# Kernel optimization log

Measured on AMD Instinct MI355X. Metric: run time of the kernel, lower is better.

## Reference

```python
import jax, jax.numpy as jnp
import numpy as np

EPS_LN = 1e-5

def layer_norm(x, w, b):
    u = x.mean(-1, keepdims=True)
    s = jnp.mean((x - u) ** 2, -1, keepdims=True)
    return w * ((x - u) / jnp.sqrt(s + EPS_LN)) + b

def mlp(x, W, b, lw, lb):
    return jax.nn.relu(layer_norm(x @ W + b, lw, lb))

def mlp_gate(x, W, b, lw, lb):
    return jax.nn.sigmoid(layer_norm(x @ W + b, lw, lb))

def setup_inputs() -> dict:
    N, D = 768, 64
    key = jax.random.key(0)
    ks = jax.random.split(key, 12)
    inp = {
        'corr_index': jax.random.normal(ks[0], (N, N, 2), jnp.float32),
        'nei_index': jax.random.randint(ks[1], (N, N), 0, 2).astype(jnp.int64),
        'nei_num': jax.random.randint(ks[2], (N,), 0, N).astype(jnp.int64),
        'hidden_state': jax.random.normal(ks[3], (N, D), jnp.float32),
        'agent_v': jax.random.normal(ks[4], (N, 2), jnp.float32),
        # relativeLayer: MLP(3, D)
        'rel_w': jax.random.normal(ks[5], (3, D), jnp.float32) * (1.0 / np.sqrt(3)),
        'rel_b': jnp.zeros((D,), jnp.float32),
        'rel_lw': jnp.ones((D,), jnp.float32),
        'rel_lb': jnp.zeros((D,), jnp.float32),
        # ngate: MLP_gate(3D, D)
        'ng_w': jax.random.normal(ks[6], (3 * D, D), jnp.float32) * (1.0 / np.sqrt(3 * D)),
        'ng_b': jnp.zeros((D,), jnp.float32),
        'ng_lw': jnp.ones((D,), jnp.float32),
        'ng_lb': jnp.zeros((D,), jnp.float32),
        # WAr: MLP(3D, 1) -- LayerNorm(1) is identity in the source
        'war_w': jax.random.normal(ks[7], (3 * D, 1), jnp.float32) * (1.0 / np.sqrt(3 * D)),
        'war_b': jnp.zeros((1,), jnp.float32),
        # weight: MLP(D, D)
        'wt_w': jax.random.normal(ks[8], (D, D), jnp.float32) * (1.0 / np.sqrt(D)),
        'wt_b': jnp.zeros((D,), jnp.float32),
        'wt_lw': jnp.ones((D,), jnp.float32),
        'wt_lb': jnp.zeros((D,), jnp.float32),
    }
    return inp

def reference(corr_index, nei_index, nei_num, hidden_state, agent_v,
              rel_w, rel_b, rel_lw, rel_lb,
              ng_w, ng_b, ng_lw, ng_lb,
              war_w, war_b,
              wt_w, wt_b, wt_lw, wt_lb):
    N, D = hidden_state.shape
    # pair layout: row i*N+j  (i = receiver row of the NxN grid, j = column)
    agent_vt = jnp.tile(agent_v, (N, 1))                     # [N*N, 2], row i*N+j -> agent_v[j]
    corr_t = corr_index.reshape(N * N, 2)
    dot = agent_vt[:, 0] * corr_t[:, 0] + agent_vt[:, 1] * corr_t[:, 1]
    judge = jnp.sum(agent_vt ** 2, -1)
    angle = dot / (jnp.sqrt(judge * jnp.sum(corr_t ** 2, -1)) + 1e-10)
    angle = jnp.where(judge == 0, -1.0, angle)
    corr3 = jnp.concatenate([corr_t, angle[:, None]], -1)    # [N*N, 3]

    r_t = mlp(corr3, rel_w, rel_b, rel_lw, rel_lb)           # [N*N, D]
    nei_inputs = jnp.tile(hidden_state, (N, 1))              # row i*N+j -> h[j]
    hi_t = jnp.repeat(hidden_state, N, axis=0)               # row i*N+j -> h[i]
    tmp = jnp.concatenate([r_t, hi_t, nei_inputs], 1)        # [N*N, 3D]

    mask = (nei_index.reshape(N * N) > 0)
    nGate = mlp_gate(tmp, ng_w, ng_b, ng_lw, ng_lb)          # [N*N, D]
    tt = jax.nn.relu(tmp @ war_w + war_b).reshape(-1)        # LayerNorm(1) == identity

    Pos = jnp.where(mask, tt, 0.0).reshape(N, N)
    Pos = jnp.where(Pos == 0, -10000.0, Pos)
    Pos = jax.nn.softmax(Pos, axis=1)
    Pos_t = Pos.reshape(-1)

    H = jnp.where(mask[:, None], nei_inputs * nGate * Pos_t[:, None], 0.0)
    H_sum = mlp(H.reshape(N, N, D).sum(1), wt_w, wt_b, wt_lw, wt_lb)
    return hidden_state + H_sum
```

## Files before the change

kernel.cpp:

```cpp
#include <hip/hip_runtime.h>
#include <math.h>

#define NN 768
#define DD 64
#define WPB 4
#define TPW (NN / 16 / WPB)
#define RSTRIDE 34
#define PREBLKS 18

typedef _Float16 half8 __attribute__((ext_vector_type(8)));
typedef float    f32x4 __attribute__((ext_vector_type(4)));
typedef __fp16   p2f   __attribute__((ext_vector_type(2)));

union FragU { uint4 u4; unsigned int u[4]; half8 h; };
union PkU   { unsigned int u; p2f p; };

__device__ __forceinline__ unsigned int pk2(float a, float b) {
    PkU t; t.p = __builtin_amdgcn_cvt_pkrtz(a, b); return t.u;
}
__device__ __forceinline__ float lane_bcast(float v, int src) {
    return __int_as_float(__builtin_amdgcn_readlane(__float_as_int(v), src));
}
__device__ __forceinline__ f32x4 mfma16(FragU a, FragU b, f32x4 c) {
    return __builtin_amdgcn_mfma_f32_16x16x32_f16(a.h, b.h, c, 0, 0, 0);
}

__global__ __launch_bounds__(256) void k_prepack(
    const float* __restrict__ hs, const float* __restrict__ ng_w,
    const float* __restrict__ ng_b, const float* __restrict__ war_w,
    const float* __restrict__ war_b,
    const float* __restrict__ rel_w, const float* __restrict__ rel_b,
    const float* __restrict__ rel_lw, const float* __restrict__ rel_lb,
    float* __restrict__ sbase, float* __restrict__ warb, float* __restrict__ war3,
    unsigned int* __restrict__ hf16,
    unsigned int* __restrict__ afragS, unsigned int* __restrict__ afragR,
    float* __restrict__ mom)
{
    const int t = threadIdx.x, blk = blockIdx.x;
    const int lane = t & 63, q = t >> 6, g = lane >> 4, c16 = lane & 15;

    if (blk >= PREBLKS) {
        const int row = (blk - PREBLKS) * 4 + q;
        const float hv = hs[row * DD + lane];
        float a2 = ng_b[lane];
        #pragma unroll 8
        for (int k = 0; k < DD; ++k)
            a2 = fmaf(lane_bcast(hv, k), ng_w[(DD + k) * DD + lane], a2);
        sbase[row * DD + lane] = a2;
        float t2 = hv * war_w[DD + lane];
        float t3 = hv * war_w[2 * DD + lane];
        #pragma unroll
        for (int o = 32; o; o >>= 1) { t2 += __shfl_xor(t2, o); t3 += __shfl_xor(t3, o); }
        if (lane == 0) { warb[row] = t2 + war_b[0]; war3[row] = t3; }
        return;
    }

    for (int idx = blk * 256 + t; idx < NN * 32; idx += PREBLKS * 256) {
        const int row = idx >> 5, c = idx & 31;
        hf16[idx] = pk2(hs[row * DD + 2 * c], hs[row * DD + 2 * c + 1]);
    }

    if (blk < 16) {
        const int b = blk >> 2, c = blk & 3;
        const int dout = 16 * b + c16;
        const int k0 = 32 * c + g * 8 + 2 * q;
        const int r0 = (k0 < 64) ? k0 : (k0 + 64);
        afragS[(blk * 64 + lane) * 4 + q] =
            pk2(ng_w[r0 * DD + dout], ng_w[(r0 + 1) * DD + dout]);
    } else if (blk == 16) {
        const int b = q;
        const int d = 16 * b + c16;
        const float rlwd = rel_lw[d], rlbd = rel_lb[d];
        const float c0 = rel_w[d] * rlwd;
        const float c1 = rel_w[DD + d] * rlwd;
        const float c2 = rel_w[2 * DD + d] * rlwd;
        const float c3 = rel_b[d] * rlwd;
        PkU h01, h23, h45;
        h01.p = __builtin_amdgcn_cvt_pkrtz(c0, c1);
        h23.p = __builtin_amdgcn_cvt_pkrtz(c2, c3);
        h45.p = __builtin_amdgcn_cvt_pkrtz(rlwd, rlbd);
        const unsigned l01 = pk2(c0 - (float)h01.p[0], c1 - (float)h01.p[1]);
        const unsigned l23 = pk2(c2 - (float)h23.p[0], c3 - (float)h23.p[1]);
        const unsigned l45 = pk2(rlwd - (float)h45.p[0], rlbd - (float)h45.p[1]);
        const unsigned int base = (b * 64 + lane) * 4;
        unsigned v0, v1, v2;
        if (g == 0 || g == 1)      { v0 = h01.u; v1 = h23.u; v2 = h45.u; }
        else if (g == 2)           { v0 = l01;   v1 = l23;   v2 = l45;   }
        else                       { v0 = 0u;    v1 = 0u;    v2 = 0u;    }
        afragR[base + 0] = v0;
        afragR[base + 1] = v1;
        afragR[base + 2] = v2;
        afragR[base + 3] = 0u;
    } else {
        if (t < 64) {
            const float x0 = rel_w[t], x1 = rel_w[DD + t], x2 = rel_w[2 * DD + t];
            const float x3 = rel_b[t];
            float v[14] = {x0, x1, x2, x3,
                           x0 * x0, x1 * x1, x2 * x2, x3 * x3,
                           x0 * x1, x0 * x2, x0 * x3, x1 * x2, x1 * x3, x2 * x3};
            #pragma unroll
            for (int qq = 0; qq < 14; ++qq) {
                float s = v[qq];
                #pragma unroll
                for (int o = 32; o; o >>= 1) s += __shfl_xor(s, o);
                if (t == 0) mom[qq] = s * (1.f / 64.f);
            }
        }
    }
}

__global__ __launch_bounds__(64 * WPB) void k_main(
    const float* __restrict__ corr, const int* __restrict__ nei,
    const float* __restrict__ hs, const float* __restrict__ av,
    const float* __restrict__ ng_lw, const float* __restrict__ ng_lb,
    const float* __restrict__ war_w,
    const float* __restrict__ sbase, const float* __restrict__ warb,
    const float* __restrict__ war3,
    const unsigned int* __restrict__ afragS, const unsigned int* __restrict__ afragR,
    const unsigned int* __restrict__ hf16, const float* __restrict__ mom,
    const float* __restrict__ wt_w, const float* __restrict__ wt_b,
    const float* __restrict__ wt_lw, const float* __restrict__ wt_lb,
    float* __restrict__ out)
{
    const int i = blockIdx.x;
    const int tid = threadIdx.x;
    const int lane = tid & 63, wave = tid >> 6;
    const int g = lane >> 4, c16 = lane & 15;

    __shared__ uint4 aSlds[16 * 64];
    __shared__ unsigned int smr[WPB * 16 * RSTRIDE];
    __shared__ float sm_red[WPB][DD];
    __shared__ float sm_m[WPB], sm_l[WPB];

    #pragma unroll
    for (int idx = tid; idx < 16 * 64; idx += 64 * WPB)
        aSlds[idx] = ((const uint4*)afragS)[idx];
    __syncthreads();

    FragU aR[4];
    #pragma unroll
    for (int b = 0; b < 4; ++b) aR[b].u4 = ((const uint4*)afragR)[b * 64 + lane];

    float sb[16], nlwv[16], nlbv[16], wv16[16];
    #pragma unroll
    for (int b = 0; b < 4; ++b)
        #pragma unroll
        for (int r = 0; r < 4; ++r) {
            const int dout = 16 * b + g * 4 + r;
            sb[b * 4 + r]   = sbase[i * DD + dout];
            nlwv[b * 4 + r] = ng_lw[dout];
            nlbv[b * 4 + r] = ng_lb[dout];
            wv16[b * 4 + r] = war_w[dout];
        }

    const float m0 = mom[0], m1 = mom[1], m2 = mom[2], m3 = mom[3];
    const float M00 = mom[4], M11 = mom[5], M22 = mom[6], M33 = mom[7];
    const float M01 = mom[8], M02 = mom[9], M03 = mom[10];
    const float M12 = mom[11], M13 = mom[12], M23 = mom[13];

    const float warbase = warb[i];
    unsigned int* wrbase = smr + (wave * 16 + c16) * RSTRIDE;

    float acc[16];
    #pragma unroll
    for (int x = 0; x < 16; ++x) acc[x] = 0.f;
    float mrun = -INFINITY, lrun = 0.f;

    int jj = 16 * wave + c16;
    float2 cc = ((const float2*)corr)[i * NN + jj];
    float2 vv = ((const float2*)av)[jj];
    int    nv = nei[i * NN + jj];
    float  w3 = war3[jj];
    FragU bx2, bx3;
    bx2.u4 = *(const uint4*)(hf16 + jj * 32 + 4 * g);
    bx3.u4 = *(const uint4*)(hf16 + jj * 32 + 16 + 4 * g);

    #pragma unroll 1
    for (int t = 0; t < TPW; ++t) {
        const f32x4 hv0 = *(const f32x4*)(hs + jj * DD +  0 + 4 * g);
        const f32x4 hv1 = *(const f32x4*)(hs + jj * DD + 16 + 4 * g);
        const f32x4 hv2 = *(const f32x4*)(hs + jj * DD + 32 + 4 * g);
        const f32x4 hv3 = *(const f32x4*)(hs + jj * DD + 48 + 4 * g);

        const int tn  = (t + 1 < TPW) ? (t + 1) : t;
        const int jjn = 16 * (wave + WPB * tn) + c16;
        const float2 cc_n = ((const float2*)corr)[i * NN + jjn];
        const float2 vv_n = ((const float2*)av)[jjn];
        const int    nv_n = nei[i * NN + jjn];
        const float  w3_n = war3[jjn];
        FragU bx2_n, bx3_n;
        bx2_n.u4 = *(const uint4*)(hf16 + jjn * 32 + 4 * g);
        bx3_n.u4 = *(const uint4*)(hf16 + jjn * 32 + 16 + 4 * g);

        const float cx = cc.x, cy = cc.y;
        const float judge = vv.x * vv.x + vv.y * vv.y;
        const float dotv = fmaf(vv.x, cx, vv.y * cy);
        const float cn = cx * cx + cy * cy;
        float angle = __fdividef(dotv, sqrtf(judge * cn) + 1e-10f);
        if (judge == 0.f) angle = -1.f;

        const float u = fmaf(cx, m0, fmaf(cy, m1, fmaf(angle, m2, m3)));
        float e2 = M33;
        e2 = fmaf(cx * cx, M00, e2);
        e2 = fmaf(cy * cy, M11, e2);
        e2 = fmaf(angle * angle, M22, e2);
        e2 = fmaf(2.f * cx, fmaf(cy, M01, fmaf(angle, M02, M03)), e2);
        e2 = fmaf(2.f * cy, fmaf(angle, M12, M13), e2);
        e2 = fmaf(2.f * angle, M23, e2);
        const float vare = (e2 - u * u) + 1e-5f;
        const float inv = rsqrtf(vare);
        const float sig = vare * inv;

        PkU s01, s23, s45;
        s01.p = __builtin_amdgcn_cvt_pkrtz(cx, cy);
        s23.p = __builtin_amdgcn_cvt_pkrtz(angle, 1.f);
        s45.p = __builtin_amdgcn_cvt_pkrtz(-u, sig);
        const unsigned l0 = pk2(cx - (float)s01.p[0], cy - (float)s01.p[1]);
        const unsigned l1 = pk2(angle - (float)s23.p[0], 0.f);
        const unsigned l2 = pk2((-u) - (float)s45.p[0], sig - (float)s45.p[1]);
        FragU b1;
        b1.u[0] = (g == 3) ? 0u : ((g == 1) ? l0 : s01.u);
        b1.u[1] = (g == 3) ? 0u : ((g == 1) ? l1 : s23.u);
        b1.u[2] = (g == 3) ? 0u : ((g == 1) ? l2 : s45.u);
        b1.u[3] = 0u;

        const f32x4 Z = {0.f, 0.f, 0.f, 0.f};
        float wd = 0.f;
        #pragma unroll
        for (int b = 0; b < 4; ++b) {
            const f32x4 P = mfma16(aR[b], b1, Z);
            const float r0f = fmaxf(P[0], 0.f) * inv;
            const float r1f = fmaxf(P[1], 0.f) * inv;
            const float r2f = fmaxf(P[2], 0.f) * inv;
            const float r3f = fmaxf(P[3], 0.f) * inv;
            wd = fmaf(r0f, wv16[b * 4 + 0], wd);
            wd = fmaf(r1f, wv16[b * 4 + 1], wd);
            wd = fmaf(r2f, wv16[b * 4 + 2], wd);
            wd = fmaf(r3f, wv16[b * 4 + 3], wd);
            uint2 wv;
            wv.x = pk2(r0f, r1f);
            wv.y = pk2(r2f, r3f);
            *(uint2*)(wrbase + 8 * b + 2 * g) = wv;
        }
        wd += __shfl_xor(wd, 16);
        wd += __shfl_xor(wd, 32);

        FragU bx0, bx1;
        {
            const uint2 lo0 = *(const uint2*)(wrbase + 4 * g);
            const uint2 hi0 = *(const uint2*)(wrbase + 4 * g + 2);
            bx0.u[0] = lo0.x; bx0.u[1] = lo0.y; bx0.u[2] = hi0.x; bx0.u[3] = hi0.y;
            const uint2 lo1 = *(const uint2*)(wrbase + 16 + 4 * g);
            const uint2 hi1 = *(const uint2*)(wrbase + 16 + 4 * g + 2);
            bx1.u[0] = lo1.x; bx1.u[1] = lo1.y; bx1.u[2] = hi1.x; bx1.u[3] = hi1.y;
        }

        f32x4 S[4];
        #pragma unroll
        for (int b = 0; b < 4; ++b) {
            FragU a0, a1, a2, a3;
            a0.u4 = aSlds[(b * 4 + 0) * 64 + lane];
            a1.u4 = aSlds[(b * 4 + 1) * 64 + lane];
            a2.u4 = aSlds[(b * 4 + 2) * 64 + lane];
            a3.u4 = aSlds[(b * 4 + 3) * 64 + lane];
            f32x4 cinit = {sb[b * 4 + 0], sb[b * 4 + 1], sb[b * 4 + 2], sb[b * 4 + 3]};
            cinit = mfma16(a0, bx0, cinit);
            cinit = mfma16(a1, bx1, cinit);
            cinit = mfma16(a2, bx2, cinit);
            cinit = mfma16(a3, bx3, cinit);
            S[b] = cinit;
        }

        float s1 = 0.f, s2 = 0.f;
        #pragma unroll
        for (int x = 0; x < 16; ++x) {
            const float sv = S[x >> 2][x & 3];
            s1 += sv; s2 = fmaf(sv, sv, s2);
        }
        s1 += __shfl_xor(s1, 16); s1 += __shfl_xor(s1, 32);
        s2 += __shfl_xor(s2, 16); s2 += __shfl_xor(s2, 32);
        const float u2 = s1 * (1.f / 64.f);
        const float var2 = fmaf(s2, 1.f / 64.f, -u2 * u2);
        const float inv2 = rsqrtf(var2 + 1e-5f);

        float tt = wd + w3 + warbase;
        tt = fmaxf(tt, 0.f);
        const bool msk = nv > 0;
        const float p = (msk && tt > 0.f) ? tt : -10000.f;

        float pm = p;
        pm = fmaxf(pm, __shfl_xor(pm, 1));
        pm = fmaxf(pm, __shfl_xor(pm, 2));
        pm = fmaxf(pm, __shfl_xor(pm, 4));
        pm = fmaxf(pm, __shfl_xor(pm, 8));
        const float mn = fmaxf(mrun, pm);
        const float alpha = __expf(mrun - mn);
        const float e = __expf(p - mn);
        const float eacc = msk ? e : 0.f;
        lrun = fmaf(lrun, alpha, e);
        mrun = mn;

        #pragma unroll
        for (int b = 0; b < 4; ++b) {
            const f32x4 hvb = (b == 0) ? hv0 : (b == 1) ? hv1 : (b == 2) ? hv2 : hv3;
            #pragma unroll
            for (int r = 0; r < 4; ++r) {
                const float ngv = fmaf((S[b][r] - u2) * inv2, nlwv[b * 4 + r],
                                       nlbv[b * 4 + r]);
                const float gate = __fdividef(1.f, 1.f + __expf(-ngv));
                acc[b * 4 + r] = fmaf(acc[b * 4 + r], alpha, eacc * gate * hvb[r]);
            }
        }

        jj = jjn; cc = cc_n; vv = vv_n; nv = nv_n; w3 = w3_n;
        bx2 = bx2_n; bx3 = bx3_n;
    }

    #pragma unroll
    for (int o = 1; o <= 8; o <<= 1) {
        lrun += __shfl_xor(lrun, o);
        #pragma unroll
        for (int x = 0; x < 16; ++x) acc[x] += __shfl_xor(acc[x], o);
    }
    if (c16 == 0) {
        #pragma unroll
        for (int b = 0; b < 4; ++b)
            #pragma unroll
            for (int r = 0; r < 4; ++r)
                sm_red[wave][16 * b + g * 4 + r] = acc[b * 4 + r];
        if (lane == 0) { sm_m[wave] = mrun; sm_l[wave] = lrun; }
    }
    __syncthreads();

    if (tid < DD) {
        float M = sm_m[0];
        #pragma unroll
        for (int w = 1; w < WPB; ++w) M = fmaxf(M, sm_m[w]);
        float L = 0.f, A = 0.f;
        #pragma unroll
        for (int w = 0; w < WPB; ++w) {
            const float f = __expf(sm_m[w] - M);
            L = fmaf(sm_l[w], f, L);
            A = fmaf(sm_red[w][tid], f, A);
        }
        const float Hv = A / L;
        float v = wt_b[tid];
        #pragma unroll 8
        for (int k = 0; k < DD; ++k)
            v = fmaf(lane_bcast(Hv, k), wt_w[k * DD + tid], v);
        float t1 = v, t2 = v * v;
        #pragma unroll
        for (int o = 32; o; o >>= 1) { t1 += __shfl_xor(t1, o); t2 += __shfl_xor(t2, o); }
        const float uo = t1 * (1.f / 64.f);
        const float varo = fmaf(t2, 1.f / 64.f, -uo * uo);
        const float invo = rsqrtf(varo + 1e-5f);
        const float ro = fmaf((v - uo) * invo, wt_lw[tid], wt_lb[tid]);
        out[i * DD + tid] = hs[i * DD + tid] + fmaxf(ro, 0.f);
    }
}

extern "C" void kernel_launch(void* const* d_in, const int* in_sizes, int n_in,
                              void* d_out, int out_size, void* d_ws, size_t ws_size,
                              hipStream_t stream) {
    const float* corr   = (const float*)d_in[0];
    const int*   nei    = (const int*)  d_in[1];
    const float* hs     = (const float*)d_in[3];
    const float* av     = (const float*)d_in[4];
    const float* rel_w  = (const float*)d_in[5];
    const float* rel_b  = (const float*)d_in[6];
    const float* rel_lw = (const float*)d_in[7];
    const float* rel_lb = (const float*)d_in[8];
    const float* ng_w   = (const float*)d_in[9];
    const float* ng_b   = (const float*)d_in[10];
    const float* ng_lw  = (const float*)d_in[11];
    const float* ng_lb  = (const float*)d_in[12];
    const float* war_w  = (const float*)d_in[13];
    const float* war_b  = (const float*)d_in[14];
    const float* wt_w   = (const float*)d_in[15];
    const float* wt_b   = (const float*)d_in[16];
    const float* wt_lw  = (const float*)d_in[17];
    const float* wt_lb  = (const float*)d_in[18];
    float* out = (float*)d_out;

    float* ws    = (float*)d_ws;
    float* sbase = ws;
    float* warb  = sbase + NN * DD;
    float* war3  = warb + NN;
    float* mom   = war3 + NN;
    unsigned int* hf16   = (unsigned int*)(mom + 16);
    unsigned int* afragS = hf16 + NN * 32;
    unsigned int* afragR = afragS + 16 * 64 * 4;

    k_prepack<<<PREBLKS + NN / 4, 256, 0, stream>>>(
        hs, ng_w, ng_b, war_w, war_b, rel_w, rel_b, rel_lw, rel_lb,
        sbase, warb, war3, hf16, afragS, afragR, mom);
    k_main<<<NN, 64 * WPB, 0, stream>>>(
        corr, nei, hs, av, ng_lw, ng_lb, war_w, sbase, warb, war3,
        afragS, afragR, hf16, mom, wt_w, wt_b, wt_lw, wt_lb, out);
}
```

Baseline: 149.2 us.

## Compute per-pair relative features once per lane and distribute via bpermute

```diff
diff --git a/kernel.cpp b/kernel.cpp
--- a/kernel.cpp
+++ b/kernel.cpp
@@ -4,7 +4,9 @@
 #define NN 768
 #define DD 64
 #define WPB 4
-#define TPW (NN / 16 / WPB)
+#define JPW (NN / WPB)
+#define NMACRO (JPW / 64)
+#define NTILES (JPW / 16)
 #define RSTRIDE 34
 #define PREBLKS 18
 
@@ -20,6 +22,12 @@
 }
 __device__ __forceinline__ float lane_bcast(float v, int src) {
     return __int_as_float(__builtin_amdgcn_readlane(__float_as_int(v), src));
+}
+__device__ __forceinline__ unsigned bperm_u(int addr, unsigned v) {
+    return (unsigned)__builtin_amdgcn_ds_bpermute(addr, (int)v);
+}
+__device__ __forceinline__ float bperm_f(int addr, float v) {
+    return __int_as_float(__builtin_amdgcn_ds_bpermute(addr, __float_as_int(v)));
 }
 __device__ __forceinline__ f32x4 mfma16(FragU a, FragU b, f32x4 c) {
     return __builtin_amdgcn_mfma_f32_16x16x32_f16(a.h, b.h, c, 0, 0, 0);
@@ -166,154 +174,185 @@
     for (int x = 0; x < 16; ++x) acc[x] = 0.f;
     float mrun = -INFINITY, lrun = 0.f;
 
-    int jj = 16 * wave + c16;
-    float2 cc = ((const float2*)corr)[i * NN + jj];
-    float2 vv = ((const float2*)av)[jj];
-    int    nv = nei[i * NN + jj];
-    float  w3 = war3[jj];
+    const int jbase = wave * JPW;
+
+    int jF = jbase + lane;
+    float2 ccF = ((const float2*)corr)[i * NN + jF];
+    float2 vvF = ((const float2*)av)[jF];
+    int    nvF = nei[i * NN + jF];
+    float  w3F = war3[jF];
+
+    int jj0 = jbase + c16;
     FragU bx2, bx3;
-    bx2.u4 = *(const uint4*)(hf16 + jj * 32 + 4 * g);
-    bx3.u4 = *(const uint4*)(hf16 + jj * 32 + 16 + 4 * g);
+    bx2.u4 = *(const uint4*)(hf16 + jj0 * 32 + 4 * g);
+    bx3.u4 = *(const uint4*)(hf16 + jj0 * 32 + 16 + 4 * g);
 
     #pragma unroll 1
-    for (int t = 0; t < TPW; ++t) {
-        const f32x4 hv0 = *(const f32x4*)(hs + jj * DD +  0 + 4 * g);
-        const f32x4 hv1 = *(const f32x4*)(hs + jj * DD + 16 + 4 * g);
-        const f32x4 hv2 = *(const f32x4*)(hs + jj * DD + 32 + 4 * g);
-        const f32x4 hv3 = *(const f32x4*)(hs + jj * DD + 48 + 4 * g);
-
-        const int tn  = (t + 1 < TPW) ? (t + 1) : t;
-        const int jjn = 16 * (wave + WPB * tn) + c16;
-        const float2 cc_n = ((const float2*)corr)[i * NN + jjn];
-        const float2 vv_n = ((const float2*)av)[jjn];
-        const int    nv_n = nei[i * NN + jjn];
-        const float  w3_n = war3[jjn];
-        FragU bx2_n, bx3_n;
-        bx2_n.u4 = *(const uint4*)(hf16 + jjn * 32 + 4 * g);
-        bx3_n.u4 = *(const uint4*)(hf16 + jjn * 32 + 16 + 4 * g);
-
-        const float cx = cc.x, cy = cc.y;
-        const float judge = vv.x * vv.x + vv.y * vv.y;
-        const float dotv = fmaf(vv.x, cx, vv.y * cy);
-        const float cn = cx * cx + cy * cy;
-        float angle = __fdividef(dotv, sqrtf(judge * cn) + 1e-10f);
-        if (judge == 0.f) angle = -1.f;
-
-        const float u = fmaf(cx, m0, fmaf(cy, m1, fmaf(angle, m2, m3)));
-        float e2 = M33;
-        e2 = fmaf(cx * cx, M00, e2);
-        e2 = fmaf(cy * cy, M11, e2);
-        e2 = fmaf(angle * angle, M22, e2);
-        e2 = fmaf(2.f * cx, fmaf(cy, M01, fmaf(angle, M02, M03)), e2);
-        e2 = fmaf(2.f * cy, fmaf(angle, M12, M13), e2);
-        e2 = fmaf(2.f * angle, M23, e2);
-        const float vare = (e2 - u * u) + 1e-5f;
-        const float inv = rsqrtf(vare);
-        const float sig = vare * inv;
-
-        PkU s01, s23, s45;
-        s01.p = __builtin_amdgcn_cvt_pkrtz(cx, cy);
-        s23.p = __builtin_amdgcn_cvt_pkrtz(angle, 1.f);
-        s45.p = __builtin_amdgcn_cvt_pkrtz(-u, sig);
-        const unsigned l0 = pk2(cx - (float)s01.p[0], cy - (float)s01.p[1]);
-        const unsigned l1 = pk2(angle - (float)s23.p[0], 0.f);
-        const unsigned l2 = pk2((-u) - (float)s45.p[0], sig - (float)s45.p[1]);
-        FragU b1;
-        b1.u[0] = (g == 3) ? 0u : ((g == 1) ? l0 : s01.u);
-        b1.u[1] = (g == 3) ? 0u : ((g == 1) ? l1 : s23.u);
-        b1.u[2] = (g == 3) ? 0u : ((g == 1) ? l2 : s45.u);
-        b1.u[3] = 0u;
-
-        const f32x4 Z = {0.f, 0.f, 0.f, 0.f};
-        float wd = 0.f;
-        #pragma unroll
-        for (int b = 0; b < 4; ++b) {
-            const f32x4 P = mfma16(aR[b], b1, Z);
-            const float r0f = fmaxf(P[0], 0.f) * inv;
-            const float r1f = fmaxf(P[1], 0.f) * inv;
-            const float r2f = fmaxf(P[2], 0.f) * inv;
-            const float r3f = fmaxf(P[3], 0.f) * inv;
-            wd = fmaf(r0f, wv16[b * 4 + 0], wd);
-            wd = fmaf(r1f, wv16[b * 4 + 1], wd);
-            wd = fmaf(r2f, wv16[b * 4 + 2], wd);
-            wd = fmaf(r3f, wv16[b * 4 + 3], wd);
-            uint2 wv;
-            wv.x = pk2(r0f, r1f);
-            wv.y = pk2(r2f, r3f);
-            *(uint2*)(wrbase + 8 * b + 2 * g) = wv;
-        }
-        wd += __shfl_xor(wd, 16);
-        wd += __shfl_xor(wd, 32);
-
-        FragU bx0, bx1;
+    for (int T = 0; T < NMACRO; ++T) {
+        unsigned FH0, FH1, FH2, FL0, FL1, FL2;
+        float FINV; int FNV; float FW3;
         {
-            const uint2 lo0 = *(const uint2*)(wrbase + 4 * g);
-            const uint2 hi0 = *(const uint2*)(wrbase + 4 * g + 2);
-            bx0.u[0] = lo0.x; bx0.u[1] = lo0.y; bx0.u[2] = hi0.x; bx0.u[3] = hi0.y;
-            const uint2 lo1 = *(const uint2*)(wrbase + 16 + 4 * g);
-            const uint2 hi1 = *(const uint2*)(wrbase + 16 + 4 * g + 2);
-            bx1.u[0] = lo1.x; bx1.u[1] = lo1.y; bx1.u[2] = hi1.x; bx1.u[3] = hi1.y;
-        }
-
-        f32x4 S[4];
-        #pragma unroll
-        for (int b = 0; b < 4; ++b) {
-            FragU a0, a1, a2, a3;
-            a0.u4 = aSlds[(b * 4 + 0) * 64 + lane];
-            a1.u4 = aSlds[(b * 4 + 1) * 64 + lane];
-            a2.u4 = aSlds[(b * 4 + 2) * 64 + lane];
-            a3.u4 = aSlds[(b * 4 + 3) * 64 + lane];
-            f32x4 cinit = {sb[b * 4 + 0], sb[b * 4 + 1], sb[b * 4 + 2], sb[b * 4 + 3]};
-            cinit = mfma16(a0, bx0, cinit);
-            cinit = mfma16(a1, bx1, cinit);
-            cinit = mfma16(a2, bx2, cinit);
-            cinit = mfma16(a3, bx3, cinit);
-            S[b] = cinit;
-        }
-
-        float s1 = 0.f, s2 = 0.f;
-        #pragma unroll
-        for (int x = 0; x < 16; ++x) {
-            const float sv = S[x >> 2][x & 3];
-            s1 += sv; s2 = fmaf(sv, sv, s2);
-        }
-        s1 += __shfl_xor(s1, 16); s1 += __shfl_xor(s1, 32);
-        s2 += __shfl_xor(s2, 16); s2 += __shfl_xor(s2, 32);
-        const float u2 = s1 * (1.f / 64.f);
-        const float var2 = fmaf(s2, 1.f / 64.f, -u2 * u2);
-        const float inv2 = rsqrtf(var2 + 1e-5f);
-
-        float tt = wd + w3 + warbase;
-        tt = fmaxf(tt, 0.f);
-        const bool msk = nv > 0;
-        const float p = (msk && tt > 0.f) ? tt : -10000.f;
-
-        float pm = p;
-        pm = fmaxf(pm, __shfl_xor(pm, 1));
-        pm = fmaxf(pm, __shfl_xor(pm, 2));
-        pm = fmaxf(pm, __shfl_xor(pm, 4));
-        pm = fmaxf(pm, __shfl_xor(pm, 8));
-        const float mn = fmaxf(mrun, pm);
-        const float alpha = __expf(mrun - mn);
-        const float e = __expf(p - mn);
-        const float eacc = msk ? e : 0.f;
-        lrun = fmaf(lrun, alpha, e);
-        mrun = mn;
-
-        #pragma unroll
-        for (int b = 0; b < 4; ++b) {
-            const f32x4 hvb = (b == 0) ? hv0 : (b == 1) ? hv1 : (b == 2) ? hv2 : hv3;
-            #pragma unroll
-            for (int r = 0; r < 4; ++r) {
-                const float ngv = fmaf((S[b][r] - u2) * inv2, nlwv[b * 4 + r],
-                                       nlbv[b * 4 + r]);
-                const float gate = __fdividef(1.f, 1.f + __expf(-ngv));
-                acc[b * 4 + r] = fmaf(acc[b * 4 + r], alpha, eacc * gate * hvb[r]);
-            }
-        }
-
-        jj = jjn; cc = cc_n; vv = vv_n; nv = nv_n; w3 = w3_n;
-        bx2 = bx2_n; bx3 = bx3_n;
+            const float cx = ccF.x, cy = ccF.y;
+            const float judge = vvF.x * vvF.x + vvF.y * vvF.y;
+            const float dotv = fmaf(vvF.x, cx, vvF.y * cy);
+            const float cn = cx * cx + cy * cy;
+            float angle = __fdividef(dotv, sqrtf(judge * cn) + 1e-10f);
+            if (judge == 0.f) angle = -1.f;
+
+            const float u = fmaf(cx, m0, fmaf(cy, m1, fmaf(angle, m2, m3)));
+            float e2 = M33;
+            e2 = fmaf(cx * cx, M00, e2);
+            e2 = fmaf(cy * cy, M11, e2);
+            e2 = fmaf(angle * angle, M22, e2);
+            e2 = fmaf(2.f * cx, fmaf(cy, M01, fmaf(angle, M02, M03)), e2);
+            e2 = fmaf(2.f * cy, fmaf(angle, M12, M13), e2);
+            e2 = fmaf(2.f * angle, M23, e2);
+            const float vare = (e2 - u * u) + 1e-5f;
+            const float inv = rsqrtf(vare);
+            const float sig = vare * inv;
+
+            PkU s01, s23, s45;
+            s01.p = __builtin_amdgcn_cvt_pkrtz(cx, cy);
+            s23.p = __builtin_amdgcn_cvt_pkrtz(angle, 1.f);
+            s45.p = __builtin_amdgcn_cvt_pkrtz(-u, sig);
+            FH0 = s01.u; FH1 = s23.u; FH2 = s45.u;
+            FL0 = pk2(cx - (float)s01.p[0], cy - (float)s01.p[1]);
+            FL1 = pk2(angle - (float)s23.p[0], 0.f);
+            FL2 = pk2((-u) - (float)s45.p[0], sig - (float)s45.p[1]);
+            FINV = inv; FNV = nvF; FW3 = w3F;
+        }
+        if (T + 1 < NMACRO) {
+            jF += 64;
+            ccF = ((const float2*)corr)[i * NN + jF];
+            vvF = ((const float2*)av)[jF];
+            nvF = nei[i * NN + jF];
+            w3F = war3[jF];
+        }
+
+        #pragma unroll 1
+        for (int s = 0; s < 4; ++s) {
+            const int jj = jbase + 64 * T + 16 * s + c16;
+
+            const f32x4 hv0 = *(const f32x4*)(hs + jj * DD +  0 + 4 * g);
+            const f32x4 hv1 = *(const f32x4*)(hs + jj * DD + 16 + 4 * g);
+            const f32x4 hv2 = *(const f32x4*)(hs + jj * DD + 32 + 4 * g);
+            const f32x4 hv3 = *(const f32x4*)(hs + jj * DD + 48 + 4 * g);
+
+            const bool last = (T == NMACRO - 1) && (s == 3);
+            const int jjn = last ? jj : jj + 16;
+            FragU bx2_n, bx3_n;
+            bx2_n.u4 = *(const uint4*)(hf16 + jjn * 32 + 4 * g);
+            bx3_n.u4 = *(const uint4*)(hf16 + jjn * 32 + 16 + 4 * g);
+
+            const int bpad = (16 * s + c16) << 2;
+            const unsigned h0 = bperm_u(bpad, FH0);
+            const unsigned h1 = bperm_u(bpad, FH1);
+            const unsigned h2 = bperm_u(bpad, FH2);
+            const unsigned l0 = bperm_u(bpad, FL0);
+            const unsigned l1 = bperm_u(bpad, FL1);
+            const unsigned l2 = bperm_u(bpad, FL2);
+            const float    invp = bperm_f(bpad, FINV);
+            const int      nvp  = (int)bperm_u(bpad, (unsigned)FNV);
+            const float    w3p  = bperm_f(bpad, FW3);
+
+            FragU b1;
+            b1.u[0] = (g == 3) ? 0u : ((g == 1) ? l0 : h0);
+            b1.u[1] = (g == 3) ? 0u : ((g == 1) ? l1 : h1);
+            b1.u[2] = (g == 3) ? 0u : ((g == 1) ? l2 : h2);
+            b1.u[3] = 0u;
+
+            const f32x4 Z = {0.f, 0.f, 0.f, 0.f};
+            float wd = 0.f;
+            #pragma unroll
+            for (int b = 0; b < 4; ++b) {
+                const f32x4 P = mfma16(aR[b], b1, Z);
+                const float r0f = fmaxf(P[0], 0.f) * invp;
+                const float r1f = fmaxf(P[1], 0.f) * invp;
+                const float r2f = fmaxf(P[2], 0.f) * invp;
+                const float r3f = fmaxf(P[3], 0.f) * invp;
+                wd = fmaf(r0f, wv16[b * 4 + 0], wd);
+                wd = fmaf(r1f, wv16[b * 4 + 1], wd);
+                wd = fmaf(r2f, wv16[b * 4 + 2], wd);
+                wd = fmaf(r3f, wv16[b * 4 + 3], wd);
+                uint2 wv;
+                wv.x = pk2(r0f, r1f);
+                wv.y = pk2(r2f, r3f);
+                *(uint2*)(wrbase + 8 * b + 2 * g) = wv;
+            }
+            wd += __shfl_xor(wd, 16);
+            wd += __shfl_xor(wd, 32);
+
+            FragU bx0, bx1;
+            {
+                const uint2 lo0 = *(const uint2*)(wrbase + 4 * g);
+                const uint2 hi0 = *(const uint2*)(wrbase + 4 * g + 2);
+                bx0.u[0] = lo0.x; bx0.u[1] = lo0.y; bx0.u[2] = hi0.x; bx0.u[3] = hi0.y;
+                const uint2 lo1 = *(const uint2*)(wrbase + 16 + 4 * g);
+                const uint2 hi1 = *(const uint2*)(wrbase + 16 + 4 * g + 2);
+                bx1.u[0] = lo1.x; bx1.u[1] = lo1.y; bx1.u[2] = hi1.x; bx1.u[3] = hi1.y;
+            }
+
+            f32x4 S[4];
+            #pragma unroll
+            for (int b = 0; b < 4; ++b) {
+                FragU a0, a1, a2, a3;
+                a0.u4 = aSlds[(b * 4 + 0) * 64 + lane];
+                a1.u4 = aSlds[(b * 4 + 1) * 64 + lane];
+                a2.u4 = aSlds[(b * 4 + 2) * 64 + lane];
+                a3.u4 = aSlds[(b * 4 + 3) * 64 + lane];
+                f32x4 cinit = {sb[b * 4 + 0], sb[b * 4 + 1],
+                               sb[b * 4 + 2], sb[b * 4 + 3]};
+                cinit = mfma16(a0, bx0, cinit);
+                cinit = mfma16(a1, bx1, cinit);
+                cinit = mfma16(a2, bx2, cinit);
+                cinit = mfma16(a3, bx3, cinit);
+                S[b] = cinit;
+            }
+
+            float s1 = 0.f, s2 = 0.f;
+            #pragma unroll
+            for (int x = 0; x < 16; ++x) {
+                const float sv = S[x >> 2][x & 3];
+                s1 += sv; s2 = fmaf(sv, sv, s2);
+            }
+            s1 += __shfl_xor(s1, 16); s1 += __shfl_xor(s1, 32);
+            s2 += __shfl_xor(s2, 16); s2 += __shfl_xor(s2, 32);
+            const float u2 = s1 * (1.f / 64.f);
+            const float var2 = fmaf(s2, 1.f / 64.f, -u2 * u2);
+            const float inv2 = rsqrtf(var2 + 1e-5f);
+
+            float tt = wd + w3p + warbase;
+            tt = fmaxf(tt, 0.f);
+            const bool msk = nvp > 0;
+            const float p = (msk && tt > 0.f) ? tt : -10000.f;
+
+            float pm = p;
+            pm = fmaxf(pm, __shfl_xor(pm, 1));
+            pm = fmaxf(pm, __shfl_xor(pm, 2));
+            pm = fmaxf(pm, __shfl_xor(pm, 4));
+            pm = fmaxf(pm, __shfl_xor(pm, 8));
+            const float mn = fmaxf(mrun, pm);
+            const float alpha = __expf(mrun - mn);
+            const float e = __expf(p - mn);
+            const float eacc = msk ? e : 0.f;
+            lrun = fmaf(lrun, alpha, e);
+            mrun = mn;
+
+            #pragma unroll
+            for (int b = 0; b < 4; ++b) {
+                const f32x4 hvb = (b == 0) ? hv0 : (b == 1) ? hv1
+                                : (b == 2) ? hv2 : hv3;
+                #pragma unroll
+                for (int r = 0; r < 4; ++r) {
+                    const float ngv = fmaf((S[b][r] - u2) * inv2, nlwv[b * 4 + r],
+                                           nlbv[b * 4 + r]);
+                    const float gate = __fdividef(1.f, 1.f + __expf(-ngv));
+                    acc[b * 4 + r] = fmaf(acc[b * 4 + r], alpha, eacc * gate * hvb[r]);
+                }
+            }
+
+            bx2 = bx2_n; bx3 = bx3_n;
+        }
     }
 
     #pragma unroll
```

Result: slower. 168.6 us (+13.0%).
